# Optimization experiments

Hardware: AMD Instinct MI355X
Metric: run time of the kernel (lower is better)

## Reference

```python
import jax, jax.numpy as jnp
import numpy as np

BT = 64  # time chunk size (matches Triton BT)


def _chunk_simple_gla(q, k, v, g):
    """Chunked simple-GLA / RWKV6c forward.
    q,k: [B,H,T,K]; v: [B,H,T,V]; g: [B,H,T] per-token log decay.
    Token-level math: S_t = exp(g_t)*S_{t-1} + k_t v_t^T ; o_t = scale * q_t @ S_t.
    Computed chunk-wise exactly as the Triton kernels do.
    """
    B, H, T, K = q.shape
    V = v.shape[-1]
    NT = T // BT
    scale = K ** -0.5

    qc = q.reshape(B, H, NT, BT, K)
    kc = k.reshape(B, H, NT, BT, K)
    vc = v.reshape(B, H, NT, BT, V)
    gc = jnp.cumsum(g.reshape(B, H, NT, BT), axis=-1)  # chunk-local cumulative log decay
    g_last = gc[..., -1]                               # [B,H,NT]

    # per-chunk kv contribution: sum_s k_s (v_s * exp(g_last - g_s))^T
    w = jnp.exp(g_last[..., None] - gc)                # [B,H,NT,BT]
    chunk_kv = jnp.einsum('bhntk,bhntv->bhnkv', kc, vc * w[..., None])
    decay = jnp.exp(g_last)                            # [B,H,NT]

    # inter-chunk state recurrence: h_n = state BEFORE chunk n
    def scan_fn(S, x):
        d, kv = x
        S_new = d[..., None, None] * S + kv
        return S_new, S  # emit state entering this chunk

    xs = (jnp.moveaxis(decay, 2, 0), jnp.moveaxis(chunk_kv, 2, 0))
    S0 = jnp.zeros((B, H, K, V), dtype=q.dtype)
    _, h = jax.lax.scan(scan_fn, S0, xs)               # h: [NT,B,H,K,V]
    h = jnp.moveaxis(h, 0, 2)                          # [B,H,NT,K,V]

    # inter-chunk output: exp(g_t) * q_t @ h_chunk * scale
    o_inter = jnp.einsum('bhntk,bhnkv->bhntv', qc, h) * jnp.exp(gc)[..., None] * scale

    # intra-chunk causal output with gated mask exp(g_i - g_j), i >= j
    s = jnp.einsum('bhnik,bhnjk->bhnij', qc, kc)
    mask = jnp.tril(jnp.ones((BT, BT), dtype=bool))
    s = jnp.where(mask, s * jnp.exp(gc[..., :, None] - gc[..., None, :]) * scale, 0.0)
    o_intra = jnp.einsum('bhnij,bhnjv->bhniv', s, vc)

    return (o_inter + o_intra).reshape(B, H, T, V)


def setup_inputs() -> dict:
    key = jax.random.key(0)
    kq, kk, kv, kg = jax.random.split(key, 4)
    B, H, T, K, V = 2, 32, 4096, 128, 128
    q = jax.random.normal(kq, (B, H, T, K), dtype=jnp.float32)
    k = jax.random.normal(kk, (B, H, T, K), dtype=jnp.float32)
    v = jax.random.normal(kv, (B, H, T, V), dtype=jnp.float32)
    # log-decay gates: negative so exp(cumsum) is bounded (RWKV6/GLA semantics)
    g = -0.5 * jax.random.uniform(kg, (B, H, T), dtype=jnp.float32)
    return {"q": q, "k": k, "v": v, "g": g}


def reference(q, k, v, g):
    return _chunk_simple_gla(q, k, v, g)
```

## Files before the change

kernel.cpp:

```cpp
#include <hip/hip_runtime.h>
#include <hip/hip_bf16.h>


#define BT 64
#define KD 128
#define VD 128
#define VSG 32
#define NCHUNK 64
#define SEGC 16
#define TLEN 4096
#define SCALE 0.08838834764831845f

#define QSTR 136
#define SHSTR 72
#define SVSTR 136
#define VTSTR 72

#define KV_PER 16384
#define KV_TOT (64 * 3 * KV_PER)
#define GS_OFF KV_TOT
#define WS_NEED ((size_t)(KV_TOT + 192) * 4)

typedef __bf16 bf16;
typedef __bf16 bf16x8 __attribute__((ext_vector_type(8)));
typedef __bf16 bf16x4 __attribute__((ext_vector_type(4)));
typedef float f32x4 __attribute__((ext_vector_type(4)));

#define MFMA __builtin_amdgcn_mfma_f32_16x16x32_bf16
#define LGKM_BARRIER() do { asm volatile("s_waitcnt lgkmcnt(0)" ::: "memory"); \
                            __builtin_amdgcn_s_barrier(); } while (0)

__device__ __forceinline__ int ksw(int t) { return ((t >> 3) & 3) << 5; }

__device__ __forceinline__ int vt_off(int vc, int t) {
  int byte = vc * (VTSTR * 2) + t * 2;
  byte ^= ((vc >> 2) & 7) << 4;
  return byte >> 1;
}

__device__ __forceinline__ bf16x8 frag_row(const bf16* p, int stride, int row0,
                                           int kk0, int lane) {
  int row = row0 + (lane & 15);
  int kk = kk0 + ((lane >> 4) << 3);
  return *(const bf16x8*)(p + row * stride + kk);
}

__device__ __forceinline__ bf16x8 krow_frag(const bf16* ks_, int row0, int kk0,
                                            int lane) {
  int row = row0 + (lane & 15);
  int kk = kk0 + ((lane >> 4) << 3);
  int byte = (row * (QSTR * 2) + kk * 2) ^ ksw(row);
  return *(const bf16x8*)((const char*)ks_ + byte);
}

__device__ __forceinline__ bf16x8 kcol_frag(const bf16* ks_, int T0, int kdA) {
  int C = ((T0 >> 3) & 3) << 5;
  int b0 = T0 * (QSTR * 2) + kdA * 2;
  bf16x8 f;
#pragma unroll
  for (int j = 0; j < 8; ++j)
    f[j] = *(const bf16*)((const char*)ks_ + ((b0 + j * (QSTR * 2)) ^ C));
  return f;
}

__device__ __forceinline__ void st4(bf16* p, float a, float b, float c, float d) {
  bf16x4 t;
  t[0] = (bf16)a; t[1] = (bf16)b; t[2] = (bf16)c; t[3] = (bf16)d;
  *(bf16x4*)p = t;
}

__device__ __forceinline__ void st8(bf16* p, const float4& a, const float4& b) {
  bf16x8 t;
  t[0] = (bf16)a.x; t[1] = (bf16)a.y; t[2] = (bf16)a.z; t[3] = (bf16)a.w;
  t[4] = (bf16)b.x; t[5] = (bf16)b.y; t[6] = (bf16)b.z; t[7] = (bf16)b.w;
  *(bf16x8*)p = t;
}

__global__ void __launch_bounds__(512, 2)
gla_pre(const float* __restrict__ kg, const float* __restrict__ vg,
        const float* __restrict__ gg, float* __restrict__ ws)
{
  __shared__ __align__(16) bf16 k_s[2][BT * QSTR];
  __shared__ __align__(16) bf16 vwT_s[2][VD * VTSTR];
  __shared__ __align__(16) float gc_all[SEGC][BT];
  __shared__ float glast_all[SEGC];

  const int tid = threadIdx.x;
  const int wave = tid >> 6;
  const int lane = tid & 63;
  const int bh = blockIdx.x & 63;
  const int sub = blockIdx.x >> 6;

  const int jc = lane & 15;
  const int g4 = lane >> 4;
  const int r0 = g4 << 2;

  const size_t kbase = (size_t)bh * TLEN * KD + (size_t)sub * 1024 * KD;
  const size_t gbase = (size_t)bh * TLEN + (size_t)sub * 1024;
  const int vrow = tid >> 3;
  const int vcq = (tid & 7) << 2;

  float4 kpf[4], vpf[4];

  auto loadall = [&](int n) {
    const float4* k4 = (const float4*)(kg + kbase + (size_t)n * (BT * KD));
    kpf[0] = k4[2 * tid];        kpf[1] = k4[2 * tid + 1];
    kpf[2] = k4[1024 + 2 * tid]; kpf[3] = k4[1024 + 2 * tid + 1];
    const float* vrp = vg + kbase + (size_t)(n * BT + vrow) * VD + vcq;
#pragma unroll
    for (int q = 0; q < 4; ++q) vpf[q] = *(const float4*)(vrp + q * 32);
  };

  auto stage = [&](int buf, int n) {
#pragma unroll
    for (int i = 0; i < 2; ++i) {
      int row = i * 32 + (tid >> 4);
      int col0 = (tid & 15) << 3;
      int byte = (row * (QSTR * 2) + col0 * 2) ^ ksw(row);
      st8((bf16*)((char*)k_s[buf] + byte), kpf[2 * i], kpf[2 * i + 1]);
    }
    bf16* vwt = vwT_s[buf];
    float wv = __expf(glast_all[n] - gc_all[n][vrow]);
#pragma unroll
    for (int q = 0; q < 4; ++q) {
      const float* vp = (const float*)&vpf[q];
#pragma unroll
      for (int e = 0; e < 4; ++e)
        vwt[vt_off(vcq + q * 32 + e, vrow)] = (bf16)(vp[e] * wv);
    }
  };

  f32x4 S[8];
#pragma unroll
  for (int a = 0; a < 8; ++a) S[a] = {0.f, 0.f, 0.f, 0.f};

  loadall(0);
#pragma unroll 1
  for (int i = 0; i < 2; ++i) {
    int cn = wave * 2 + i;
    float a = gg[gbase + cn * BT + lane];
#pragma unroll
    for (int off = 1; off < 64; off <<= 1) {
      float t = __shfl_up(a, off);
      if (lane >= off) a += t;
    }
    gc_all[cn][lane] = a;
    if (lane == 63) glast_all[cn] = a;
  }
  LGKM_BARRIER();
  stage(0, 0);
  loadall(1);
  LGKM_BARRIER();

#pragma unroll 1
  for (int n = 0; n < SEGC; ++n) {
    const int cur = n & 1;
    float dec = __expf(glast_all[n]);
#pragma unroll
    for (int a = 0; a < 8; ++a) S[a] *= dec;
#pragma unroll
    for (int ks = 0; ks < 2; ++ks) {
      bf16x8 ka = kcol_frag(k_s[cur], ks * 32 + (g4 << 3), wave * 16 + jc);
#pragma unroll
      for (int a = 0; a < 8; ++a) {
        bf16x8 b = *(const bf16x8*)(vwT_s[cur] + vt_off(16 * a + jc, ks * 32 + (g4 << 3)));
        S[a] = MFMA(ka, b, S[a], 0, 0, 0);
      }
    }
    if (n + 1 < SEGC) {
      stage(cur ^ 1, n + 1);
      if (n + 2 < SEGC) loadall(n + 2);
    }
    LGKM_BARRIER();
  }

  float* kv = ws + ((size_t)bh * 3 + sub) * KV_PER;
#pragma unroll
  for (int a = 0; a < 8; ++a)
#pragma unroll
    for (int r = 0; r < 4; ++r)
      kv[(wave * 16 + r0 + r) * VD + 16 * a + jc] = S[a][r];
  if (tid == 0) {
    float gs = 0.f;
    for (int n = 0; n < SEGC; ++n) gs += glast_all[n];
    ws[GS_OFF + bh * 3 + sub] = gs;
  }
}

__global__ void __launch_bounds__(512, 2)
gla_main(const float* __restrict__ qg, const float* __restrict__ kg,
         const float* __restrict__ vg, const float* __restrict__ gg,
         float* __restrict__ og, const float* __restrict__ ws)
{
  __shared__ __align__(16) bf16 q_s[BT * QSTR];
  __shared__ __align__(16) bf16 k_s[BT * QSTR];
  __shared__ __align__(16) bf16 vT_s[2][VD * VTSTR];
  __shared__ __align__(16) bf16 vwT_s[2][VD * VTSTR];
  __shared__ __align__(16) bf16 sh_s[BT * SHSTR];
  __shared__ __align__(16) bf16 svt_s[VD * SVSTR];
  __shared__ __align__(16) float gc_all[SEGC][BT];
  __shared__ float glast_all[SEGC];

  const int tid = threadIdx.x;
  const int wave = tid >> 6;
  const int lane = tid & 63;
  const int bh = blockIdx.x & 63;
  const int seg = blockIdx.x >> 6;

  const int jc = lane & 15;
  const int g4 = lane >> 4;
  const int r0 = g4 << 2;

  const int it = wave & 3;
  const int jt0 = (wave < 4) ? 0 : 2;
  const int vq0 = (wave >> 2) << 2;

  const size_t qkbase = (size_t)bh * TLEN * KD + (size_t)seg * 1024 * KD;
  const size_t gbase = (size_t)bh * TLEN + (size_t)seg * 1024;
  const int vrow = tid >> 3;
  const int vcq = (tid & 7) << 2;

  float4 qpf[4], kpf[4], vpf[4];

  auto loadall = [&](int n) {
    const float4* q4 = (const float4*)(qg + qkbase + (size_t)n * (BT * KD));
    const float4* k4 = (const float4*)(kg + qkbase + (size_t)n * (BT * KD));
    qpf[0] = q4[2 * tid];        qpf[1] = q4[2 * tid + 1];
    qpf[2] = q4[1024 + 2 * tid]; qpf[3] = q4[1024 + 2 * tid + 1];
    kpf[0] = k4[2 * tid];        kpf[1] = k4[2 * tid + 1];
    kpf[2] = k4[1024 + 2 * tid]; kpf[3] = k4[1024 + 2 * tid + 1];
    const float* vrp = vg + qkbase + (size_t)(n * BT + vrow) * VD + vcq;
#pragma unroll
    for (int q = 0; q < 4; ++q) vpf[q] = *(const float4*)(vrp + q * 32);
  };

  auto stage = [&](int vbuf, int n) {
#pragma unroll
    for (int i = 0; i < 2; ++i) {
      int row = i * 32 + (tid >> 4);
      int col0 = (tid & 15) << 3;
      st8(&q_s[row * QSTR + col0], qpf[2 * i], qpf[2 * i + 1]);
      int byte = (row * (QSTR * 2) + col0 * 2) ^ ksw(row);
      st8((bf16*)((char*)k_s + byte), kpf[2 * i], kpf[2 * i + 1]);
    }
    bf16* vt = vT_s[vbuf];
    bf16* vwt = vwT_s[vbuf];
    float wv = __expf(glast_all[n] - gc_all[n][vrow]);
#pragma unroll
    for (int q = 0; q < 4; ++q) {
      const float* vp = (const float*)&vpf[q];
#pragma unroll
      for (int e = 0; e < 4; ++e) {
        int vc = vcq + q * 32 + e;
        vt[vt_off(vc, vrow)] = (bf16)vp[e];
        vwt[vt_off(vc, vrow)] = (bf16)(vp[e] * wv);
      }
    }
  };

  f32x4 S[8];
#pragma unroll
  for (int a = 0; a < 8; ++a) S[a] = {0.f, 0.f, 0.f, 0.f};

  if (seg > 0) {
    float D1 = __expf(ws[GS_OFF + bh * 3 + 1]);
    float D2 = __expf(ws[GS_OFF + bh * 3 + 2]);
    float mult[3];
    mult[0] = (seg == 1) ? 1.f : ((seg == 2) ? D1 : D1 * D2);
    mult[1] = (seg == 2) ? 1.f : D2;
    mult[2] = 1.f;
    for (int j = 0; j < seg && j < 3; ++j) {
      const float* kv = ws + ((size_t)bh * 3 + j) * KV_PER;
      float m = mult[j];
#pragma unroll
      for (int a = 0; a < 8; ++a)
#pragma unroll
        for (int r = 0; r < 4; ++r)
          S[a][r] += m * kv[(wave * 16 + r0 + r) * VD + 16 * a + jc];
    }
  }

  loadall(0);
#pragma unroll 1
  for (int i = 0; i < 2; ++i) {
    int cn = wave * 2 + i;
    float a = gg[gbase + cn * BT + lane];
#pragma unroll
    for (int off = 1; off < 64; off <<= 1) {
      float t = __shfl_up(a, off);
      if (lane >= off) a += t;
    }
    gc_all[cn][lane] = a;
    if (lane == 63) glast_all[cn] = a;
  }
  LGKM_BARRIER();
  stage(0, 0);
  loadall(1);
  LGKM_BARRIER();

#pragma unroll 1
  for (int n = 0; n < SEGC; ++n) {
    const int cur = n & 1;

    bf16x8 af[4];
#pragma unroll
    for (int ks = 0; ks < 4; ++ks)
      af[ks] = frag_row(q_s, QSTR, it * 16, ks * 32, lane);

    f32x4 sa0 = {0.f,0.f,0.f,0.f}, sa1 = {0.f,0.f,0.f,0.f};
#pragma unroll
    for (int ks = 0; ks < 4; ++ks) {
      bf16x8 a0 = krow_frag(k_s, jt0 * 16, ks * 32, lane);
      bf16x8 a1 = krow_frag(k_s, (jt0 + 1) * 16, ks * 32, lane);
      sa0 = MFMA(a0, af[ks], sa0, 0, 0, 0);
      sa1 = MFMA(a1, af[ks], sa1, 0, 0, 0);
    }
    {
      int i0 = it * 16 + jc;
      float gci = gc_all[n][i0];
#pragma unroll
      for (int t = 0; t < 2; ++t) {
        f32x4 sv = t ? sa1 : sa0;
        int jb = (jt0 + t) * 16 + r0;
        float4 g4v = *(const float4*)&gc_all[n][jb];
        const float* gj = (const float*)&g4v;
        bf16x4 pk;
#pragma unroll
        for (int r = 0; r < 4; ++r) {
          float val = (i0 >= jb + r) ? sv[r] * __expf(gci - gj[r]) * SCALE : 0.f;
          pk[r] = (bf16)val;
        }
        *(bf16x4*)&sh_s[i0 * SHSTR + jb] = pk;
      }
    }

#pragma unroll
    for (int a = 0; a < 8; ++a)
      st4(&svt_s[(16 * a + jc) * SVSTR + wave * 16 + r0],
          S[a][0], S[a][1], S[a][2], S[a][3]);

    if (n + 1 < SEGC) {
      float dec = __expf(glast_all[n]);
#pragma unroll
      for (int a = 0; a < 8; ++a) S[a] *= dec;
#pragma unroll
      for (int ks = 0; ks < 2; ++ks) {
        bf16x8 ka = kcol_frag(k_s, ks * 32 + (g4 << 3), wave * 16 + jc);
#pragma unroll
        for (int a = 0; a < 8; ++a) {
          bf16x8 b = *(const bf16x8*)(vwT_s[cur] + vt_off(16 * a + jc, ks * 32 + (g4 << 3)));
          S[a] = MFMA(ka, b, S[a], 0, 0, 0);
        }
      }
    }
    LGKM_BARRIER();

    {
      bf16x8 sha[2];
#pragma unroll
      for (int ks = 0; ks < 2; ++ks)
        sha[ks] = frag_row(sh_s, SHSTR, it * 16, ks * 32, lane);
      float eg[4];
      {
        float4 e4 = *(const float4*)&gc_all[n][it * 16 + r0];
        const float* ep = (const float*)&e4;
#pragma unroll
        for (int r = 0; r < 4; ++r) eg[r] = __expf(ep[r]) * SCALE;
      }
#pragma unroll
      for (int p = 0; p < 4; ++p) {
        int vq = vq0 + p;
        f32x4 oacc = {0.f, 0.f, 0.f, 0.f};
#pragma unroll
        for (int ks = 0; ks < 4; ++ks) {
          bf16x8 b = frag_row(svt_s, SVSTR, vq * 16, ks * 32, lane);
          oacc = MFMA(af[ks], b, oacc, 0, 0, 0);
        }
#pragma unroll
        for (int r = 0; r < 4; ++r) oacc[r] *= eg[r];
#pragma unroll
        for (int ks = 0; ks < 2; ++ks) {
          bf16x8 b = *(const bf16x8*)(vT_s[cur] + vt_off(vq * 16 + jc, ks * 32 + (g4 << 3)));
          oacc = MFMA(sha[ks], b, oacc, 0, 0, 0);
        }
#pragma unroll
        for (int r = 0; r < 4; ++r) {
          int row = it * 16 + r0 + r;
          og[qkbase + (size_t)(n * BT + row) * VD + vq * 16 + jc] = oacc[r];
        }
      }
    }
    if (n + 1 < SEGC) {
      stage(cur ^ 1, n + 1);
      if (n + 2 < SEGC) loadall(n + 2);
    }
    LGKM_BARRIER();
  }
}

__global__ void __launch_bounds__(512, 2)
gla_fused(const float* __restrict__ qg, const float* __restrict__ kg,
          const float* __restrict__ vg, const float* __restrict__ gg,
          float* __restrict__ og)
{
  __shared__ __align__(16) bf16 q_s[2][BT * QSTR];
  __shared__ __align__(16) bf16 k_s[2][BT * QSTR];
  __shared__ __align__(16) bf16 vT_s[3][VSG * VTSTR];
  __shared__ __align__(16) bf16 vwT_s[3][VSG * VTSTR];
  __shared__ __align__(16) bf16 sh_s[2][BT * SHSTR];
  __shared__ __align__(16) bf16 svt_s[2][VSG * SVSTR];
  __shared__ __align__(16) float gc_all[NCHUNK][BT];
  __shared__ float glast_all[NCHUNK];

  const int tid = threadIdx.x;
  const int wave = tid >> 6;
  const int lane = tid & 63;
  const int bh = blockIdx.x & 63;
  const int vseg = blockIdx.x >> 6;

  const int jc = lane & 15;
  const int g4 = lane >> 4;
  const int r0 = g4 << 2;

  const int it = wave & 3;
  const int nt = wave >> 2;
  const int jt0 = (wave < 4) ? 0 : 2;

  const size_t qkbase = (size_t)bh * TLEN * KD;
  const size_t gbase = (size_t)bh * TLEN;
  const size_t vbase = (size_t)bh * TLEN * VD + (size_t)vseg * VSG;
  const int vrow = tid >> 3;
  const int vc0 = (tid & 7) << 2;

  float4 qpf[4], kpf[4], vpf;

  auto loadpf = [&](int n) {
    const float4* q4 = (const float4*)(qg + qkbase + (size_t)n * (BT * KD));
    const float4* k4 = (const float4*)(kg + qkbase + (size_t)n * (BT * KD));
#pragma unroll
    for (int i = 0; i < 4; ++i) { qpf[i] = q4[i * 512 + tid]; kpf[i] = k4[i * 512 + tid]; }
    vpf = *(const float4*)(vg + vbase + (size_t)(n * BT + vrow) * VD + vc0);
  };

  auto stage = [&](int b2, int b3, int n) {
#pragma unroll
    for (int i = 0; i < 4; ++i) {
      int f4 = i * 512 + tid;
      int t = f4 >> 5;
      int kd0 = (f4 & 31) << 2;
      st4(&q_s[b2][t * QSTR + kd0], qpf[i].x, qpf[i].y, qpf[i].z, qpf[i].w);
      int byte = (t * (QSTR * 2) + kd0 * 2) ^ ksw(t);
      st4((bf16*)((char*)k_s[b2] + byte), kpf[i].x, kpf[i].y, kpf[i].z, kpf[i].w);
    }
    bf16* vt = vT_s[b3];
    bf16* vwt = vwT_s[b3];
    float wv = __expf(glast_all[n] - gc_all[n][vrow]);
    vt[vt_off(vc0 + 0, vrow)] = (bf16)vpf.x;
    vt[vt_off(vc0 + 1, vrow)] = (bf16)vpf.y;
    vt[vt_off(vc0 + 2, vrow)] = (bf16)vpf.z;
    vt[vt_off(vc0 + 3, vrow)] = (bf16)vpf.w;
    vwt[vt_off(vc0 + 0, vrow)] = (bf16)(vpf.x * wv);
    vwt[vt_off(vc0 + 1, vrow)] = (bf16)(vpf.y * wv);
    vwt[vt_off(vc0 + 2, vrow)] = (bf16)(vpf.z * wv);
    vwt[vt_off(vc0 + 3, vrow)] = (bf16)(vpf.w * wv);
  };

  auto o_emit = [&](int no, int b2o, int b3o, const bf16x8 (&afp)[4]) {
    f32x4 oacc = {0.f, 0.f, 0.f, 0.f};
#pragma unroll
    for (int ks = 0; ks < 4; ++ks) {
      bf16x8 b = frag_row(svt_s[b2o], SVSTR, nt * 16, ks * 32, lane);
      oacc = MFMA(afp[ks], b, oacc, 0, 0, 0);
    }
    {
      float4 e4 = *(const float4*)&gc_all[no][it * 16 + r0];
      const float* ep = (const float*)&e4;
#pragma unroll
      for (int r = 0; r < 4; ++r) oacc[r] *= __expf(ep[r]) * SCALE;
    }
#pragma unroll
    for (int ks = 0; ks < 2; ++ks) {
      bf16x8 a = frag_row(sh_s[b2o], SHSTR, it * 16, ks * 32, lane);
      bf16x8 b = *(const bf16x8*)(vT_s[b3o] + vt_off(nt * 16 + jc, ks * 32 + (g4 << 3)));
      oacc = MFMA(a, b, oacc, 0, 0, 0);
    }
#pragma unroll
    for (int r = 0; r < 4; ++r) {
      int row = it * 16 + r0 + r;
      og[vbase + (size_t)(no * BT + row) * VD + nt * 16 + jc] = oacc[r];
    }
  };

  f32x4 Sa = {0.f, 0.f, 0.f, 0.f}, Sb = {0.f, 0.f, 0.f, 0.f};
  bf16x8 afp[4];

  loadpf(0);
#pragma unroll 1
  for (int i = 0; i < 8; ++i) {
    int cn = wave * 8 + i;
    float a = gg[gbase + cn * BT + lane];
#pragma unroll
    for (int off = 1; off < 64; off <<= 1) {
      float t = __shfl_up(a, off);
      if (lane >= off) a += t;
    }
    gc_all[cn][lane] = a;
    if (lane == 63) glast_all[cn] = a;
  }
  LGKM_BARRIER();
  stage(0, 0, 0);
  loadpf(1);
  LGKM_BARRIER();

  int b3 = 0;
#pragma unroll 1
  for (int n = 0; n < NCHUNK; ++n) {
    const int b2 = n & 1;
    const int b3n = (b3 == 2) ? 0 : b3 + 1;
    const int b3p = (b3 == 0) ? 2 : b3 - 1;

    if (n > 0) o_emit(n - 1, b2 ^ 1, b3p, afp);

    bf16x8 af[4];
#pragma unroll
    for (int ks = 0; ks < 4; ++ks)
      af[ks] = frag_row(q_s[b2], QSTR, it * 16, ks * 32, lane);

    f32x4 sa0 = {0.f,0.f,0.f,0.f}, sa1 = {0.f,0.f,0.f,0.f};
#pragma unroll
    for (int ks = 0; ks < 4; ++ks) {
      bf16x8 a0 = krow_frag(k_s[b2], jt0 * 16, ks * 32, lane);
      bf16x8 a1 = krow_frag(k_s[b2], (jt0 + 1) * 16, ks * 32, lane);
      sa0 = MFMA(a0, af[ks], sa0, 0, 0, 0);
      sa1 = MFMA(a1, af[ks], sa1, 0, 0, 0);
    }
    {
      int i0 = it * 16 + jc;
      float gci = gc_all[n][i0];
#pragma unroll
      for (int t = 0; t < 2; ++t) {
        f32x4 sv = t ? sa1 : sa0;
        int jb = (jt0 + t) * 16 + r0;
        float4 g4v = *(const float4*)&gc_all[n][jb];
        const float* gj = (const float*)&g4v;
        bf16x4 pk;
#pragma unroll
        for (int r = 0; r < 4; ++r) {
          float val = (i0 >= jb + r) ? sv[r] * __expf(gci - gj[r]) * SCALE : 0.f;
          pk[r] = (bf16)val;
        }
        *(bf16x4*)&sh_s[b2][i0 * SHSTR + jb] = pk;
      }
    }

    st4(&svt_s[b2][jc * SVSTR + wave * 16 + r0], Sa[0], Sa[1], Sa[2], Sa[3]);
    st4(&svt_s[b2][(16 + jc) * SVSTR + wave * 16 + r0], Sb[0], Sb[1], Sb[2], Sb[3]);
    {
      float dec = __expf(glast_all[n]);
#pragma unroll
      for (int r = 0; r < 4; ++r) { Sa[r] *= dec; Sb[r] *= dec; }
#pragma unroll
      for (int ks = 0; ks < 2; ++ks) {
        bf16x8 a = kcol_frag(k_s[b2], ks * 32 + (g4 << 3), wave * 16 + jc);
        bf16x8 b0 = *(const bf16x8*)(vwT_s[b3] + vt_off(jc, ks * 32 + (g4 << 3)));
        bf16x8 b1 = *(const bf16x8*)(vwT_s[b3] + vt_off(16 + jc, ks * 32 + (g4 << 3)));
        Sa = MFMA(a, b0, Sa, 0, 0, 0);
        Sb = MFMA(a, b1, Sb, 0, 0, 0);
      }
    }

    if (n + 1 < NCHUNK) {
      stage(b2 ^ 1, b3n, n + 1);
      if (n + 2 < NCHUNK) loadpf(n + 2);
    }

#pragma unroll
    for (int ks = 0; ks < 4; ++ks) afp[ks] = af[ks];
    b3 = b3n;

    LGKM_BARRIER();
  }

  o_emit(NCHUNK - 1, 1, 0, afp);
}

extern "C" void kernel_launch(void* const* d_in, const int* in_sizes, int n_in,
                              void* d_out, int out_size, void* d_ws, size_t ws_size,
                              hipStream_t stream) {
  const float* q = (const float*)d_in[0];
  const float* k = (const float*)d_in[1];
  const float* v = (const float*)d_in[2];
  const float* g = (const float*)d_in[3];
  float* o = (float*)d_out;
  if (ws_size >= WS_NEED) {
    float* ws = (float*)d_ws;
    gla_pre<<<dim3(192), dim3(512), 0, stream>>>(k, v, g, ws);
    gla_main<<<dim3(256), dim3(512), 0, stream>>>(q, k, v, g, o, ws);
  } else {
    gla_fused<<<dim3(256), dim3(512), 0, stream>>>(q, k, v, g, o);
  }
}
```

Baseline: 171.1 us.

## Split prepass into 6 parts and double main kernel threads to 1024

The prepass now computes chunk KV partial states over 8-chunk parts (6 parts per head) instead of 16-chunk parts, doubling grid parallelism and shortening its serial loop. The main kernel uses 1024 threads per block so each wave owns a quarter of the state (K-tile by V-half), one score tile, and two output tiles, and it combines prior partial states with running decay products. This reduces per-thread register pressure and per-wave serial work, at the cost of more waves per block contending on barriers and shared memory. Launch bounds are raised for both kernels.

Result: slower. 197.5 us (+15.5%).

```diff
diff --git a/kernel.cpp b/kernel.cpp
--- a/kernel.cpp
+++ b/kernel.cpp
@@ -8,6 +8,8 @@
 #define VSG 32
 #define NCHUNK 64
 #define SEGC 16
+#define PREC 8
+#define NPART 6
 #define TLEN 4096
 #define SCALE 0.08838834764831845f
 
@@ -17,9 +19,9 @@
 #define VTSTR 72
 
 #define KV_PER 16384
-#define KV_TOT (64 * 3 * KV_PER)
+#define KV_TOT (64 * NPART * KV_PER)
 #define GS_OFF KV_TOT
-#define WS_NEED ((size_t)(KV_TOT + 192) * 4)
+#define WS_NEED ((size_t)(KV_TOT + 64 * NPART) * 4)
 
 typedef __bf16 bf16;
 typedef __bf16 bf16x8 __attribute__((ext_vector_type(8)));
@@ -76,27 +78,27 @@
   *(bf16x8*)p = t;
 }
 
-__global__ void __launch_bounds__(512, 2)
+__global__ void __launch_bounds__(512, 4)
 gla_pre(const float* __restrict__ kg, const float* __restrict__ vg,
         const float* __restrict__ gg, float* __restrict__ ws)
 {
   __shared__ __align__(16) bf16 k_s[2][BT * QSTR];
   __shared__ __align__(16) bf16 vwT_s[2][VD * VTSTR];
-  __shared__ __align__(16) float gc_all[SEGC][BT];
-  __shared__ float glast_all[SEGC];
+  __shared__ __align__(16) float gc_all[PREC][BT];
+  __shared__ float glast_all[PREC];
 
   const int tid = threadIdx.x;
   const int wave = tid >> 6;
   const int lane = tid & 63;
   const int bh = blockIdx.x & 63;
-  const int sub = blockIdx.x >> 6;
+  const int part = blockIdx.x >> 6;
 
   const int jc = lane & 15;
   const int g4 = lane >> 4;
   const int r0 = g4 << 2;
 
-  const size_t kbase = (size_t)bh * TLEN * KD + (size_t)sub * 1024 * KD;
-  const size_t gbase = (size_t)bh * TLEN + (size_t)sub * 1024;
+  const size_t kbase = (size_t)bh * TLEN * KD + (size_t)part * (PREC * BT) * KD;
+  const size_t gbase = (size_t)bh * TLEN + (size_t)part * (PREC * BT);
   const int vrow = tid >> 3;
   const int vcq = (tid & 7) << 2;
 
@@ -135,17 +137,15 @@
   for (int a = 0; a < 8; ++a) S[a] = {0.f, 0.f, 0.f, 0.f};
 
   loadall(0);
-#pragma unroll 1
-  for (int i = 0; i < 2; ++i) {
-    int cn = wave * 2 + i;
-    float a = gg[gbase + cn * BT + lane];
+  {
+    float a = gg[gbase + wave * BT + lane];
 #pragma unroll
     for (int off = 1; off < 64; off <<= 1) {
       float t = __shfl_up(a, off);
       if (lane >= off) a += t;
     }
-    gc_all[cn][lane] = a;
-    if (lane == 63) glast_all[cn] = a;
+    gc_all[wave][lane] = a;
+    if (lane == 63) glast_all[wave] = a;
   }
   LGKM_BARRIER();
   stage(0, 0);
@@ -153,7 +153,7 @@
   LGKM_BARRIER();
 
 #pragma unroll 1
-  for (int n = 0; n < SEGC; ++n) {
+  for (int n = 0; n < PREC; ++n) {
     const int cur = n & 1;
     float dec = __expf(glast_all[n]);
 #pragma unroll
@@ -167,14 +167,14 @@
         S[a] = MFMA(ka, b, S[a], 0, 0, 0);
       }
     }
-    if (n + 1 < SEGC) {
+    if (n + 1 < PREC) {
       stage(cur ^ 1, n + 1);
-      if (n + 2 < SEGC) loadall(n + 2);
+      if (n + 2 < PREC) loadall(n + 2);
     }
     LGKM_BARRIER();
   }
 
-  float* kv = ws + ((size_t)bh * 3 + sub) * KV_PER;
+  float* kv = ws + ((size_t)bh * NPART + part) * KV_PER;
 #pragma unroll
   for (int a = 0; a < 8; ++a)
 #pragma unroll
@@ -182,12 +182,12 @@
       kv[(wave * 16 + r0 + r) * VD + 16 * a + jc] = S[a][r];
   if (tid == 0) {
     float gs = 0.f;
-    for (int n = 0; n < SEGC; ++n) gs += glast_all[n];
-    ws[GS_OFF + bh * 3 + sub] = gs;
-  }
-}
-
-__global__ void __launch_bounds__(512, 2)
+    for (int n = 0; n < PREC; ++n) gs += glast_all[n];
+    ws[GS_OFF + bh * NPART + part] = gs;
+  }
+}
+
+__global__ void __launch_bounds__(1024, 4)
 gla_main(const float* __restrict__ qg, const float* __restrict__ kg,
          const float* __restrict__ vg, const float* __restrict__ gg,
          float* __restrict__ og, const float* __restrict__ ws)
@@ -212,86 +212,78 @@
   const int r0 = g4 << 2;
 
   const int it = wave & 3;
-  const int jt0 = (wave < 4) ? 0 : 2;
-  const int vq0 = (wave >> 2) << 2;
+  const int jt = wave >> 2;
+  const int vq0 = (wave >> 2) << 1;
+  const int kt = wave & 7;
+  const int vh = wave >> 3;
 
   const size_t qkbase = (size_t)bh * TLEN * KD + (size_t)seg * 1024 * KD;
   const size_t gbase = (size_t)bh * TLEN + (size_t)seg * 1024;
-  const int vrow = tid >> 3;
-  const int vcq = (tid & 7) << 2;
-
-  float4 qpf[4], kpf[4], vpf[4];
+  const int vrow = tid >> 4;
+  const int vc0 = (tid & 15) << 3;
+
+  float4 qpf[2], kpf[2], vpf[2];
 
   auto loadall = [&](int n) {
     const float4* q4 = (const float4*)(qg + qkbase + (size_t)n * (BT * KD));
     const float4* k4 = (const float4*)(kg + qkbase + (size_t)n * (BT * KD));
-    qpf[0] = q4[2 * tid];        qpf[1] = q4[2 * tid + 1];
-    qpf[2] = q4[1024 + 2 * tid]; qpf[3] = q4[1024 + 2 * tid + 1];
-    kpf[0] = k4[2 * tid];        kpf[1] = k4[2 * tid + 1];
-    kpf[2] = k4[1024 + 2 * tid]; kpf[3] = k4[1024 + 2 * tid + 1];
-    const float* vrp = vg + qkbase + (size_t)(n * BT + vrow) * VD + vcq;
-#pragma unroll
-    for (int q = 0; q < 4; ++q) vpf[q] = *(const float4*)(vrp + q * 32);
+    qpf[0] = q4[2 * tid]; qpf[1] = q4[2 * tid + 1];
+    kpf[0] = k4[2 * tid]; kpf[1] = k4[2 * tid + 1];
+    const float* vrp = vg + qkbase + (size_t)(n * BT + vrow) * VD + vc0;
+    vpf[0] = *(const float4*)vrp;
+    vpf[1] = *(const float4*)(vrp + 4);
   };
 
   auto stage = [&](int vbuf, int n) {
-#pragma unroll
-    for (int i = 0; i < 2; ++i) {
-      int row = i * 32 + (tid >> 4);
-      int col0 = (tid & 15) << 3;
-      st8(&q_s[row * QSTR + col0], qpf[2 * i], qpf[2 * i + 1]);
-      int byte = (row * (QSTR * 2) + col0 * 2) ^ ksw(row);
-      st8((bf16*)((char*)k_s + byte), kpf[2 * i], kpf[2 * i + 1]);
-    }
+    st8(&q_s[vrow * QSTR + vc0], qpf[0], qpf[1]);
+    int byte = (vrow * (QSTR * 2) + vc0 * 2) ^ ksw(vrow);
+    st8((bf16*)((char*)k_s + byte), kpf[0], kpf[1]);
     bf16* vt = vT_s[vbuf];
     bf16* vwt = vwT_s[vbuf];
     float wv = __expf(glast_all[n] - gc_all[n][vrow]);
 #pragma unroll
-    for (int q = 0; q < 4; ++q) {
-      const float* vp = (const float*)&vpf[q];
+    for (int h = 0; h < 2; ++h) {
+      const float* vp = (const float*)&vpf[h];
 #pragma unroll
       for (int e = 0; e < 4; ++e) {
-        int vc = vcq + q * 32 + e;
+        int vc = vc0 + h * 4 + e;
         vt[vt_off(vc, vrow)] = (bf16)vp[e];
         vwt[vt_off(vc, vrow)] = (bf16)(vp[e] * wv);
       }
     }
   };
 
-  f32x4 S[8];
-#pragma unroll
-  for (int a = 0; a < 8; ++a) S[a] = {0.f, 0.f, 0.f, 0.f};
+  f32x4 S[4];
+#pragma unroll
+  for (int a = 0; a < 4; ++a) S[a] = {0.f, 0.f, 0.f, 0.f};
 
   if (seg > 0) {
-    float D1 = __expf(ws[GS_OFF + bh * 3 + 1]);
-    float D2 = __expf(ws[GS_OFF + bh * 3 + 2]);
-    float mult[3];
-    mult[0] = (seg == 1) ? 1.f : ((seg == 2) ? D1 : D1 * D2);
-    mult[1] = (seg == 2) ? 1.f : D2;
-    mult[2] = 1.f;
-    for (int j = 0; j < seg && j < 3; ++j) {
-      const float* kv = ws + ((size_t)bh * 3 + j) * KV_PER;
-      float m = mult[j];
-#pragma unroll
-      for (int a = 0; a < 8; ++a)
-#pragma unroll
-        for (int r = 0; r < 4; ++r)
-          S[a][r] += m * kv[(wave * 16 + r0 + r) * VD + 16 * a + jc];
+    const int np = 2 * seg;
+    float run = 1.f;
+    for (int p = np - 1; p >= 0; --p) {
+      const float* kv = ws + ((size_t)bh * NPART + p) * KV_PER;
+      float gsp = ws[GS_OFF + bh * NPART + p];
+#pragma unroll
+      for (int a = 0; a < 4; ++a)
+#pragma unroll
+        for (int r = 0; r < 4; ++r) {
+          int kd = kt * 16 + r0 + r;
+          S[a][r] += run * kv[kd * VD + vh * 64 + a * 16 + jc];
+        }
+      run *= __expf(gsp);
     }
   }
 
   loadall(0);
-#pragma unroll 1
-  for (int i = 0; i < 2; ++i) {
-    int cn = wave * 2 + i;
-    float a = gg[gbase + cn * BT + lane];
+  {
+    float a = gg[gbase + wave * BT + lane];
 #pragma unroll
     for (int off = 1; off < 64; off <<= 1) {
       float t = __shfl_up(a, off);
       if (lane >= off) a += t;
     }
-    gc_all[cn][lane] = a;
-    if (lane == 63) glast_all[cn] = a;
+    gc_all[wave][lane] = a;
+    if (lane == 63) glast_all[wave] = a;
   }
   LGKM_BARRIER();
   stage(0, 0);
@@ -307,48 +299,42 @@
     for (int ks = 0; ks < 4; ++ks)
       af[ks] = frag_row(q_s, QSTR, it * 16, ks * 32, lane);
 
-    f32x4 sa0 = {0.f,0.f,0.f,0.f}, sa1 = {0.f,0.f,0.f,0.f};
-#pragma unroll
-    for (int ks = 0; ks < 4; ++ks) {
-      bf16x8 a0 = krow_frag(k_s, jt0 * 16, ks * 32, lane);
-      bf16x8 a1 = krow_frag(k_s, (jt0 + 1) * 16, ks * 32, lane);
-      sa0 = MFMA(a0, af[ks], sa0, 0, 0, 0);
-      sa1 = MFMA(a1, af[ks], sa1, 0, 0, 0);
-    }
     {
+      f32x4 sa = {0.f, 0.f, 0.f, 0.f};
+#pragma unroll
+      for (int ks = 0; ks < 4; ++ks) {
+        bf16x8 a0 = krow_frag(k_s, jt * 16, ks * 32, lane);
+        sa = MFMA(a0, af[ks], sa, 0, 0, 0);
+      }
       int i0 = it * 16 + jc;
       float gci = gc_all[n][i0];
-#pragma unroll
-      for (int t = 0; t < 2; ++t) {
-        f32x4 sv = t ? sa1 : sa0;
-        int jb = (jt0 + t) * 16 + r0;
-        float4 g4v = *(const float4*)&gc_all[n][jb];
-        const float* gj = (const float*)&g4v;
-        bf16x4 pk;
-#pragma unroll
-        for (int r = 0; r < 4; ++r) {
-          float val = (i0 >= jb + r) ? sv[r] * __expf(gci - gj[r]) * SCALE : 0.f;
-          pk[r] = (bf16)val;
-        }
-        *(bf16x4*)&sh_s[i0 * SHSTR + jb] = pk;
-      }
-    }
-
-#pragma unroll
-    for (int a = 0; a < 8; ++a)
-      st4(&svt_s[(16 * a + jc) * SVSTR + wave * 16 + r0],
+      int jb = jt * 16 + r0;
+      float4 g4v = *(const float4*)&gc_all[n][jb];
+      const float* gj = (const float*)&g4v;
+      bf16x4 pk;
+#pragma unroll
+      for (int r = 0; r < 4; ++r) {
+        float val = (i0 >= jb + r) ? sa[r] * __expf(gci - gj[r]) * SCALE : 0.f;
+        pk[r] = (bf16)val;
+      }
+      *(bf16x4*)&sh_s[i0 * SHSTR + jb] = pk;
+    }
+
+#pragma unroll
+    for (int a = 0; a < 4; ++a)
+      st4(&svt_s[(vh * 64 + a * 16 + jc) * SVSTR + kt * 16 + r0],
           S[a][0], S[a][1], S[a][2], S[a][3]);
 
     if (n + 1 < SEGC) {
       float dec = __expf(glast_all[n]);
 #pragma unroll
-      for (int a = 0; a < 8; ++a) S[a] *= dec;
+      for (int a = 0; a < 4; ++a) S[a] *= dec;
 #pragma unroll
       for (int ks = 0; ks < 2; ++ks) {
-        bf16x8 ka = kcol_frag(k_s, ks * 32 + (g4 << 3), wave * 16 + jc);
-#pragma unroll
-        for (int a = 0; a < 8; ++a) {
-          bf16x8 b = *(const bf16x8*)(vwT_s[cur] + vt_off(16 * a + jc, ks * 32 + (g4 << 3)));
+        bf16x8 ka = kcol_frag(k_s, ks * 32 + (g4 << 3), kt * 16 + jc);
+#pragma unroll
+        for (int a = 0; a < 4; ++a) {
+          bf16x8 b = *(const bf16x8*)(vwT_s[cur] + vt_off(vh * 64 + a * 16 + jc, ks * 32 + (g4 << 3)));
           S[a] = MFMA(ka, b, S[a], 0, 0, 0);
         }
       }
@@ -368,7 +354,7 @@
         for (int r = 0; r < 4; ++r) eg[r] = __expf(ep[r]) * SCALE;
       }
 #pragma unroll
-      for (int p = 0; p < 4; ++p) {
+      for (int p = 0; p < 2; ++p) {
         int vq = vq0 + p;
         f32x4 oacc = {0.f, 0.f, 0.f, 0.f};
 #pragma unroll
@@ -594,8 +580,8 @@
   float* o = (float*)d_out;
   if (ws_size >= WS_NEED) {
     float* ws = (float*)d_ws;
-    gla_pre<<<dim3(192), dim3(512), 0, stream>>>(k, v, g, ws);
-    gla_main<<<dim3(256), dim3(512), 0, stream>>>(q, k, v, g, o, ws);
+    gla_pre<<<dim3(64 * NPART), dim3(512), 0, stream>>>(k, v, g, ws);
+    gla_main<<<dim3(256), dim3(1024), 0, stream>>>(q, k, v, g, o, ws);
   } else {
     gla_fused<<<dim3(256), dim3(512), 0, stream>>>(q, k, v, g, o);
   }
```

## Merge pre and main kernels into one cooperative kernel with grid sync

Applied to the files above, without the earlier changes.

Replaces the two-launch scheme (a pre-pass computing per-segment KV state, then the main pass) with a single cooperative kernel. All 256 blocks first compute their segment's KV contribution, publish it to the workspace and pass a grid-wide barrier, then combine the preceding segments' states and run the output phase. The KV update now uses a transposed, decay-weighted K layout loaded column-wise, so the K column fragment read changes. This removes a kernel launch and lets the pre-pass use all 256 blocks, but it recomputes the segment KV in the first phase, adds a grid barrier, and needs all 256 blocks to be co-resident.

Measured after the change: 274.2 us. +60.3%, slower.

```diff
diff --git a/kernel.cpp b/kernel.cpp
--- a/kernel.cpp
+++ b/kernel.cpp
@@ -1,5 +1,8 @@
 #include <hip/hip_runtime.h>
 #include <hip/hip_bf16.h>
+#include <hip/hip_cooperative_groups.h>
+
+namespace cg = cooperative_groups;
 
 
 #define BT 64
@@ -17,9 +20,8 @@
 #define VTSTR 72
 
 #define KV_PER 16384
-#define KV_TOT (64 * 3 * KV_PER)
-#define GS_OFF KV_TOT
-#define WS_NEED ((size_t)(KV_TOT + 192) * 4)
+#define GS_OFF (64 * 3 * KV_PER)
+#define WS_NEED ((size_t)(64 * 3 * KV_PER + 192) * 4)
 
 typedef __bf16 bf16;
 typedef __bf16 bf16x8 __attribute__((ext_vector_type(8)));
@@ -32,9 +34,9 @@
 
 __device__ __forceinline__ int ksw(int t) { return ((t >> 3) & 3) << 5; }
 
-__device__ __forceinline__ int vt_off(int vc, int t) {
-  int byte = vc * (VTSTR * 2) + t * 2;
-  byte ^= ((vc >> 2) & 7) << 4;
+__device__ __forceinline__ int vt_off(int row, int t) {
+  int byte = row * (VTSTR * 2) + t * 2;
+  byte ^= ((row >> 2) & 7) << 4;
   return byte >> 1;
 }
 
@@ -77,125 +79,14 @@
 }
 
 __global__ void __launch_bounds__(512, 2)
-gla_pre(const float* __restrict__ kg, const float* __restrict__ vg,
-        const float* __restrict__ gg, float* __restrict__ ws)
-{
-  __shared__ __align__(16) bf16 k_s[2][BT * QSTR];
-  __shared__ __align__(16) bf16 vwT_s[2][VD * VTSTR];
-  __shared__ __align__(16) float gc_all[SEGC][BT];
-  __shared__ float glast_all[SEGC];
-
-  const int tid = threadIdx.x;
-  const int wave = tid >> 6;
-  const int lane = tid & 63;
-  const int bh = blockIdx.x & 63;
-  const int sub = blockIdx.x >> 6;
-
-  const int jc = lane & 15;
-  const int g4 = lane >> 4;
-  const int r0 = g4 << 2;
-
-  const size_t kbase = (size_t)bh * TLEN * KD + (size_t)sub * 1024 * KD;
-  const size_t gbase = (size_t)bh * TLEN + (size_t)sub * 1024;
-  const int vrow = tid >> 3;
-  const int vcq = (tid & 7) << 2;
-
-  float4 kpf[4], vpf[4];
-
-  auto loadall = [&](int n) {
-    const float4* k4 = (const float4*)(kg + kbase + (size_t)n * (BT * KD));
-    kpf[0] = k4[2 * tid];        kpf[1] = k4[2 * tid + 1];
-    kpf[2] = k4[1024 + 2 * tid]; kpf[3] = k4[1024 + 2 * tid + 1];
-    const float* vrp = vg + kbase + (size_t)(n * BT + vrow) * VD + vcq;
-#pragma unroll
-    for (int q = 0; q < 4; ++q) vpf[q] = *(const float4*)(vrp + q * 32);
-  };
-
-  auto stage = [&](int buf, int n) {
-#pragma unroll
-    for (int i = 0; i < 2; ++i) {
-      int row = i * 32 + (tid >> 4);
-      int col0 = (tid & 15) << 3;
-      int byte = (row * (QSTR * 2) + col0 * 2) ^ ksw(row);
-      st8((bf16*)((char*)k_s[buf] + byte), kpf[2 * i], kpf[2 * i + 1]);
-    }
-    bf16* vwt = vwT_s[buf];
-    float wv = __expf(glast_all[n] - gc_all[n][vrow]);
-#pragma unroll
-    for (int q = 0; q < 4; ++q) {
-      const float* vp = (const float*)&vpf[q];
-#pragma unroll
-      for (int e = 0; e < 4; ++e)
-        vwt[vt_off(vcq + q * 32 + e, vrow)] = (bf16)(vp[e] * wv);
-    }
-  };
-
-  f32x4 S[8];
-#pragma unroll
-  for (int a = 0; a < 8; ++a) S[a] = {0.f, 0.f, 0.f, 0.f};
-
-  loadall(0);
-#pragma unroll 1
-  for (int i = 0; i < 2; ++i) {
-    int cn = wave * 2 + i;
-    float a = gg[gbase + cn * BT + lane];
-#pragma unroll
-    for (int off = 1; off < 64; off <<= 1) {
-      float t = __shfl_up(a, off);
-      if (lane >= off) a += t;
-    }
-    gc_all[cn][lane] = a;
-    if (lane == 63) glast_all[cn] = a;
-  }
-  LGKM_BARRIER();
-  stage(0, 0);
-  loadall(1);
-  LGKM_BARRIER();
-
-#pragma unroll 1
-  for (int n = 0; n < SEGC; ++n) {
-    const int cur = n & 1;
-    float dec = __expf(glast_all[n]);
-#pragma unroll
-    for (int a = 0; a < 8; ++a) S[a] *= dec;
-#pragma unroll
-    for (int ks = 0; ks < 2; ++ks) {
-      bf16x8 ka = kcol_frag(k_s[cur], ks * 32 + (g4 << 3), wave * 16 + jc);
-#pragma unroll
-      for (int a = 0; a < 8; ++a) {
-        bf16x8 b = *(const bf16x8*)(vwT_s[cur] + vt_off(16 * a + jc, ks * 32 + (g4 << 3)));
-        S[a] = MFMA(ka, b, S[a], 0, 0, 0);
-      }
-    }
-    if (n + 1 < SEGC) {
-      stage(cur ^ 1, n + 1);
-      if (n + 2 < SEGC) loadall(n + 2);
-    }
-    LGKM_BARRIER();
-  }
-
-  float* kv = ws + ((size_t)bh * 3 + sub) * KV_PER;
-#pragma unroll
-  for (int a = 0; a < 8; ++a)
-#pragma unroll
-    for (int r = 0; r < 4; ++r)
-      kv[(wave * 16 + r0 + r) * VD + 16 * a + jc] = S[a][r];
-  if (tid == 0) {
-    float gs = 0.f;
-    for (int n = 0; n < SEGC; ++n) gs += glast_all[n];
-    ws[GS_OFF + bh * 3 + sub] = gs;
-  }
-}
-
-__global__ void __launch_bounds__(512, 2)
-gla_main(const float* __restrict__ qg, const float* __restrict__ kg,
+gla_coop(const float* __restrict__ qg, const float* __restrict__ kg,
          const float* __restrict__ vg, const float* __restrict__ gg,
-         float* __restrict__ og, const float* __restrict__ ws)
+         float* __restrict__ og, float* __restrict__ ws)
 {
   __shared__ __align__(16) bf16 q_s[BT * QSTR];
   __shared__ __align__(16) bf16 k_s[BT * QSTR];
+  __shared__ __align__(16) bf16 kwT_s[2][KD * VTSTR];
   __shared__ __align__(16) bf16 vT_s[2][VD * VTSTR];
-  __shared__ __align__(16) bf16 vwT_s[2][VD * VTSTR];
   __shared__ __align__(16) bf16 sh_s[BT * SHSTR];
   __shared__ __align__(16) bf16 svt_s[VD * SVSTR];
   __shared__ __align__(16) float gc_all[SEGC][BT];
@@ -214,73 +105,81 @@
   const int it = wave & 3;
   const int jt0 = (wave < 4) ? 0 : 2;
   const int vq0 = (wave >> 2) << 2;
-
-  const size_t qkbase = (size_t)bh * TLEN * KD + (size_t)seg * 1024 * KD;
-  const size_t gbase = (size_t)bh * TLEN + (size_t)seg * 1024;
-  const int vrow = tid >> 3;
-  const int vcq = (tid & 7) << 2;
-
-  float4 qpf[4], kpf[4], vpf[4];
-
-  auto loadall = [&](int n) {
-    const float4* q4 = (const float4*)(qg + qkbase + (size_t)n * (BT * KD));
-    const float4* k4 = (const float4*)(kg + qkbase + (size_t)n * (BT * KD));
-    qpf[0] = q4[2 * tid];        qpf[1] = q4[2 * tid + 1];
-    qpf[2] = q4[1024 + 2 * tid]; qpf[3] = q4[1024 + 2 * tid + 1];
-    kpf[0] = k4[2 * tid];        kpf[1] = k4[2 * tid + 1];
-    kpf[2] = k4[1024 + 2 * tid]; kpf[3] = k4[1024 + 2 * tid + 1];
-    const float* vrp = vg + qkbase + (size_t)(n * BT + vrow) * VD + vcq;
-#pragma unroll
-    for (int q = 0; q < 4; ++q) vpf[q] = *(const float4*)(vrp + q * 32);
-  };
-
-  auto stage = [&](int vbuf, int n) {
+  const int kt = wave;
+
+  const size_t base = (size_t)bh * TLEN * KD + (size_t)seg * (SEGC * BT) * KD;
+  const size_t gbase = (size_t)bh * TLEN + (size_t)seg * (SEGC * BT);
+
+  const int c0 = (lane) << 1;
+  const int t0 = wave << 3;
+
+  float2 kc[8], vc[8];
+  float4 qpf[4], kpf[4];
+
+  auto load_cols = [&](int n) {
+    const float* kp = kg + base + (size_t)(n * BT + t0) * KD + c0;
+    const float* vp = vg + base + (size_t)(n * BT + t0) * KD + c0;
+#pragma unroll
+    for (int i = 0; i < 8; ++i) {
+      kc[i] = *(const float2*)(kp + i * KD);
+      vc[i] = *(const float2*)(vp + i * KD);
+    }
+  };
+  auto stage_cv = [&](int buf, int n) {
+    float gl = glast_all[n];
+    bf16x8 kw0, kw1, v0, v1;
+#pragma unroll
+    for (int i = 0; i < 8; ++i) {
+      float w = __expf(gl - gc_all[n][t0 + i]);
+      kw0[i] = (bf16)(kc[i].x * w);
+      kw1[i] = (bf16)(kc[i].y * w);
+      v0[i] = (bf16)vc[i].x;
+      v1[i] = (bf16)vc[i].y;
+    }
+    *(bf16x8*)(kwT_s[buf] + vt_off(c0, t0)) = kw0;
+    *(bf16x8*)(kwT_s[buf] + vt_off(c0 + 1, t0)) = kw1;
+    *(bf16x8*)(vT_s[buf] + vt_off(c0, t0)) = v0;
+    *(bf16x8*)(vT_s[buf] + vt_off(c0 + 1, t0)) = v1;
+  };
+  auto load_rows = [&](int n) {
+    const float4* q4 = (const float4*)(qg + base + (size_t)n * (BT * KD));
+    const float4* k4 = (const float4*)(kg + base + (size_t)n * (BT * KD));
+    qpf[0] = q4[2*tid]; qpf[1] = q4[2*tid+1];
+    qpf[2] = q4[1024+2*tid]; qpf[3] = q4[1024+2*tid+1];
+    kpf[0] = k4[2*tid]; kpf[1] = k4[2*tid+1];
+    kpf[2] = k4[1024+2*tid]; kpf[3] = k4[1024+2*tid+1];
+  };
+  auto stage_qk = [&]() {
 #pragma unroll
     for (int i = 0; i < 2; ++i) {
       int row = i * 32 + (tid >> 4);
       int col0 = (tid & 15) << 3;
-      st8(&q_s[row * QSTR + col0], qpf[2 * i], qpf[2 * i + 1]);
+      st8(&q_s[row * QSTR + col0], qpf[2*i], qpf[2*i+1]);
       int byte = (row * (QSTR * 2) + col0 * 2) ^ ksw(row);
-      st8((bf16*)((char*)k_s + byte), kpf[2 * i], kpf[2 * i + 1]);
-    }
-    bf16* vt = vT_s[vbuf];
-    bf16* vwt = vwT_s[vbuf];
-    float wv = __expf(glast_all[n] - gc_all[n][vrow]);
-#pragma unroll
-    for (int q = 0; q < 4; ++q) {
-      const float* vp = (const float*)&vpf[q];
-#pragma unroll
-      for (int e = 0; e < 4; ++e) {
-        int vc = vcq + q * 32 + e;
-        vt[vt_off(vc, vrow)] = (bf16)vp[e];
-        vwt[vt_off(vc, vrow)] = (bf16)(vp[e] * wv);
+      st8((bf16*)((char*)k_s + byte), kpf[2*i], kpf[2*i+1]);
+    }
+  };
+
+  f32x4 S[8];
+#pragma unroll
+  for (int a = 0; a < 8; ++a) S[a] = {0.f, 0.f, 0.f, 0.f};
+
+  auto update = [&](int cur, int n) {
+    float dec = __expf(glast_all[n]);
+#pragma unroll
+    for (int a = 0; a < 8; ++a) S[a] *= dec;
+#pragma unroll
+    for (int ks = 0; ks < 2; ++ks) {
+      bf16x8 ka = *(const bf16x8*)(kwT_s[cur] + vt_off(kt * 16 + jc, ks * 32 + (g4 << 3)));
+#pragma unroll
+      for (int a = 0; a < 8; ++a) {
+        bf16x8 vb = *(const bf16x8*)(vT_s[cur] + vt_off(16 * a + jc, ks * 32 + (g4 << 3)));
+        S[a] = MFMA(ka, vb, S[a], 0, 0, 0);
       }
     }
   };
 
-  f32x4 S[8];
-#pragma unroll
-  for (int a = 0; a < 8; ++a) S[a] = {0.f, 0.f, 0.f, 0.f};
-
-  if (seg > 0) {
-    float D1 = __expf(ws[GS_OFF + bh * 3 + 1]);
-    float D2 = __expf(ws[GS_OFF + bh * 3 + 2]);
-    float mult[3];
-    mult[0] = (seg == 1) ? 1.f : ((seg == 2) ? D1 : D1 * D2);
-    mult[1] = (seg == 2) ? 1.f : D2;
-    mult[2] = 1.f;
-    for (int j = 0; j < seg && j < 3; ++j) {
-      const float* kv = ws + ((size_t)bh * 3 + j) * KV_PER;
-      float m = mult[j];
-#pragma unroll
-      for (int a = 0; a < 8; ++a)
-#pragma unroll
-        for (int r = 0; r < 4; ++r)
-          S[a][r] += m * kv[(wave * 16 + r0 + r) * VD + 16 * a + jc];
-    }
-  }
-
-  loadall(0);
+  load_cols(0);
 #pragma unroll 1
   for (int i = 0; i < 2; ++i) {
     int cn = wave * 2 + i;
@@ -294,8 +193,56 @@
     if (lane == 63) glast_all[cn] = a;
   }
   LGKM_BARRIER();
-  stage(0, 0);
-  loadall(1);
+  stage_cv(0, 0);
+  load_cols(1);
+  LGKM_BARRIER();
+
+#pragma unroll 1
+  for (int n = 0; n < SEGC; ++n) {
+    int cur = n & 1;
+    if (n + 1 < SEGC) stage_cv(cur ^ 1, n + 1);
+    update(cur, n);
+    if (n + 2 < SEGC) load_cols(n + 2);
+    LGKM_BARRIER();
+  }
+
+  if (seg < 3) {
+    float* kv = ws + ((size_t)bh * 3 + seg) * KV_PER;
+#pragma unroll
+    for (int a = 0; a < 8; ++a)
+#pragma unroll
+      for (int r = 0; r < 4; ++r)
+        kv[(kt * 16 + r0 + r) * VD + 16 * a + jc] = S[a][r];
+    if (tid == 0) {
+      float gs = 0.f;
+      for (int nn = 0; nn < SEGC; ++nn) gs += glast_all[nn];
+      ws[GS_OFF + bh * 3 + seg] = gs;
+    }
+  }
+  __threadfence();
+  cg::this_grid().sync();
+
+#pragma unroll
+  for (int a = 0; a < 8; ++a) S[a] = {0.f, 0.f, 0.f, 0.f};
+  if (seg > 0) {
+    float gs[3];
+#pragma unroll
+    for (int j = 0; j < 3; ++j) gs[j] = ws[GS_OFF + bh * 3 + j];
+    float m = 1.f;
+    for (int p = seg - 1; p >= 0; --p) {
+      const float* kv = ws + ((size_t)bh * 3 + p) * KV_PER;
+#pragma unroll
+      for (int a = 0; a < 8; ++a)
+#pragma unroll
+        for (int r = 0; r < 4; ++r)
+          S[a][r] += m * kv[(kt * 16 + r0 + r) * VD + 16 * a + jc];
+      m *= __expf(gs[p]);
+    }
+  }
+
+  load_rows(0); load_cols(0);
+  stage_qk(); stage_cv(0, 0);
+  load_rows(1); load_cols(1);
   LGKM_BARRIER();
 
 #pragma unroll 1
@@ -336,23 +283,10 @@
 
 #pragma unroll
     for (int a = 0; a < 8; ++a)
-      st4(&svt_s[(16 * a + jc) * SVSTR + wave * 16 + r0],
+      st4(&svt_s[(16 * a + jc) * SVSTR + kt * 16 + r0],
           S[a][0], S[a][1], S[a][2], S[a][3]);
 
-    if (n + 1 < SEGC) {
-      float dec = __expf(glast_all[n]);
-#pragma unroll
-      for (int a = 0; a < 8; ++a) S[a] *= dec;
-#pragma unroll
-      for (int ks = 0; ks < 2; ++ks) {
-        bf16x8 ka = kcol_frag(k_s, ks * 32 + (g4 << 3), wave * 16 + jc);
-#pragma unroll
-        for (int a = 0; a < 8; ++a) {
-          bf16x8 b = *(const bf16x8*)(vwT_s[cur] + vt_off(16 * a + jc, ks * 32 + (g4 << 3)));
-          S[a] = MFMA(ka, b, S[a], 0, 0, 0);
-        }
-      }
-    }
+    if (n + 1 < SEGC) update(cur, n);
     LGKM_BARRIER();
 
     {
@@ -386,13 +320,14 @@
 #pragma unroll
         for (int r = 0; r < 4; ++r) {
           int row = it * 16 + r0 + r;
-          og[qkbase + (size_t)(n * BT + row) * VD + vq * 16 + jc] = oacc[r];
+          og[base + (size_t)(n * BT + row) * VD + vq * 16 + jc] = oacc[r];
         }
       }
     }
     if (n + 1 < SEGC) {
-      stage(cur ^ 1, n + 1);
-      if (n + 2 < SEGC) loadall(n + 2);
+      stage_qk();
+      stage_cv(cur ^ 1, n + 1);
+      if (n + 2 < SEGC) { load_rows(n + 2); load_cols(n + 2); }
     }
     LGKM_BARRIER();
   }
@@ -594,8 +529,8 @@
   float* o = (float*)d_out;
   if (ws_size >= WS_NEED) {
     float* ws = (float*)d_ws;
-    gla_pre<<<dim3(192), dim3(512), 0, stream>>>(k, v, g, ws);
-    gla_main<<<dim3(256), dim3(512), 0, stream>>>(q, k, v, g, o, ws);
+    void* args[6] = {(void*)&q, (void*)&k, (void*)&v, (void*)&g, (void*)&o, (void*)&ws};
+    hipLaunchCooperativeKernel((void*)gla_coop, dim3(256), dim3(512), args, 0, stream);
   } else {
     gla_fused<<<dim3(256), dim3(512), 0, stream>>>(q, k, v, g, o);
   }
```
